# Kernel optimization log

Measured on AMD Instinct MI355X. Metric: run time of the kernel, lower is better.

The kernel has to match this reference:

```python
import jax, jax.numpy as jnp
import numpy as np

B, S, D = 2, 8192, 1024
H, DK, DV = 8, 64, 64
DH = 4096
SEG = 2048
NSEG = S // SEG
EPS = 1e-5


def setup_inputs() -> dict:
    key = jax.random.key(0)
    ks = jax.random.split(key, 9)
    g = lambda k, shp, sc: jax.random.normal(k, shp, jnp.float32) * sc
    return {
        "x": g(ks[0], (B, S, D), 1.0),
        "Wq": g(ks[1], (D, H * DK), 0.02),
        "Wk": g(ks[2], (D, H * DK), 0.02),
        "Wv": g(ks[3], (D, H * DV), 0.02),
        "Wo": g(ks[4], (H * DV, D), 0.02),
        "betas": g(ks[5], (1, H, 1, DV), 1.0),
        "W1": g(ks[6], (D, DH), 0.02),
        "b1": jnp.zeros((DH,), jnp.float32),
        "W2": g(ks[7], (DH, D), 0.02),
        "b2": jnp.zeros((D,), jnp.float32),
        "ln_g": jnp.ones((D,), jnp.float32),
        "ln_b": jnp.zeros((D,), jnp.float32),
    }


def _compressive_memory(x, Wq, Wk, Wv, Wo, betas):
    # project and split heads: (B, H, S, d)
    q = (x @ Wq).reshape(B, S, H, DK).transpose(0, 2, 1, 3)
    k = (x @ Wk).reshape(B, S, H, DK).transpose(0, 2, 1, 3)
    v = (x @ Wv).reshape(B, S, H, DV).transpose(0, 2, 1, 3)

    # chunk into segments: (NSEG, B, H, SEG, d)
    seg = lambda t, d: t.reshape(B, H, NSEG, SEG, d).transpose(2, 0, 1, 3, 4)
    qs, ks_, vs = seg(q, DK), seg(k, DK), seg(v, DV)

    mem0 = jnp.zeros((B, H, DK, DV), jnp.float32)
    z0 = jnp.ones((B, H, DK, 1), jnp.float32) / DK
    causal_mask = jnp.tril(jnp.ones((SEG, SEG), bool))
    scale = np.float32(1.0 / np.sqrt(DK))
    gate = jax.nn.sigmoid(betas)  # (1, H, 1, DV)

    def step(carry, inp):
        mem, z = carry
        qi, ki, vi = inp  # (B, H, SEG, d)
        sq = jax.nn.elu(qi) + 1.0
        sk = jax.nn.elu(ki) + 1.0
        # memory retrieval (uses state from previous segments)
        att_mem = (sq @ mem) / (sq @ z)  # (B, H, SEG, DV)
        # local causal SDP attention within the segment
        scores = jnp.einsum('bhqd,bhkd->bhqk', qi, ki) * scale
        scores = jnp.where(causal_mask, scores, -jnp.inf)
        att_dot = jax.nn.softmax(scores, axis=-1) @ vi
        # linear memory update
        mem = mem + jnp.einsum('bhsd,bhsv->bhdv', sk, vi)
        z = z + sk.sum(axis=-2, keepdims=True).transpose(0, 1, 3, 2)
        att = gate * att_mem + (1.0 - gate) * att_dot
        return (mem, z), att

    _, atts = jax.lax.scan(step, (mem0, z0), (qs, ks_, vs))
    # (NSEG, B, H, SEG, DV) -> (B, S, H*DV)
    att = atts.transpose(1, 0, 3, 2, 4).reshape(B, S, H * DV)
    return att @ Wo


def reference(x, Wq, Wk, Wv, Wo, betas, W1, b1, W2, b2, ln_g, ln_b):
    a = _compressive_memory(x, Wq, Wk, Wv, Wo, betas)
    h = jax.nn.gelu(a @ W1 + b1, approximate=False) @ W2 + b2
    y = h + x
    mu = y.mean(axis=-1, keepdims=True)
    var = ((y - mu) ** 2).mean(axis=-1, keepdims=True)
    return (y - mu) / jnp.sqrt(var + EPS) * ln_g + ln_b
```

## Files before the change

kernel.cpp:

```cpp
#include <hip/hip_runtime.h>
#include <hip/hip_bf16.h>
#include <math.h>

#define B_    2
#define S_    8192
#define D_    1024
#define H_N   8
#define DK_   64
#define DV_   64
#define DH_   4096
#define SEG_  2048
#define NSEG_ 4
#define EPS_  1e-5f
#define LDQKV 1536

typedef __hip_bfloat16 bf16;
typedef unsigned int u32;
typedef __attribute__((ext_vector_type(8))) short bf16x8;
typedef __attribute__((ext_vector_type(4))) float f32x4;

union bvec { bf16x8 v; bf16 e[8]; };

template <typename T> __device__ inline T from_f(float v);
template <> __device__ inline float from_f<float>(float v) { return v; }
template <> __device__ inline bf16  from_f<bf16>(float v)  { return __float2bfloat16(v); }

__device__ __forceinline__ void gld_lds16(const bf16* g, bf16* l) {
    __builtin_amdgcn_global_load_lds(
        (const __attribute__((address_space(1))) u32*)g,
        (__attribute__((address_space(3))) u32*)l, 16, 0, 0);
}

__device__ inline float elu1(float x) { return x > 0.f ? x + 1.f : __expf(x); }

template <int EPI, typename CT>
__global__ __launch_bounds__(512, 2) void gemm256(
    const bf16* __restrict__ A, const bf16* __restrict__ BT, CT* __restrict__ C,
    const float* __restrict__ bias, const float* __restrict__ resid,
    int M, int N, int K)
{
    __shared__ bf16 L[2][32768];
    const int t    = threadIdx.x;
    const int lane = t & 63;
    const int w    = t >> 6;
    const int la   = lane & 15;
    const int g    = lane >> 4;

    const int nx  = gridDim.x;
    const int nwg = nx * gridDim.y;
    const int lin = blockIdx.y * nx + blockIdx.x;
    const int swz = (lin & 7) * (nwg >> 3) + (lin >> 3);
    const int by  = swz / nx, bx = swz - by * nx;

    const int m0 = by * 256, n0 = bx * 256;
    const int wm = w >> 2, wn = w & 3;

    f32x4 acc[8][4];
    #pragma unroll
    for (int m = 0; m < 8; m++)
        #pragma unroll
        for (int n = 0; n < 4; n++) {
            f32x4 z4 = {0.f, 0.f, 0.f, 0.f};
            acc[m][n] = z4;
        }

    const bf16* Aw = A  + (size_t)(m0 + w * 32) * K;
    const bf16* Bw = BT + (size_t)(n0 + w * 32) * K;
    const int sr = lane >> 3;
    const int sc = ((lane & 7) ^ sr) * 8;

    const int nt = K >> 6;

    auto stage = [&](int kt) {
        const int buf = kt & 1;
        const size_t k0 = (size_t)kt << 6;
        #pragma unroll
        for (int i = 0; i < 4; i++) {
            gld_lds16(Aw + (size_t)(i * 8 + sr) * K + k0 + sc,
                      &L[buf][(w * 32 + i * 8) * 64]);
            gld_lds16(Bw + (size_t)(i * 8 + sr) * K + k0 + sc,
                      &L[buf][16384 + (w * 32 + i * 8) * 64]);
        }
    };

    auto rd = [&](const bf16* base, int row, int chunk) -> bf16x8 {
        return *(const bf16x8*)((const char*)base + row * 128 + ((chunk ^ (row & 7)) << 4));
    };

    stage(0);
    asm volatile("s_waitcnt vmcnt(0)" ::: "memory");
    __builtin_amdgcn_sched_barrier(0);
    __builtin_amdgcn_s_barrier();
    __builtin_amdgcn_sched_barrier(0);

    for (int kt = 0; kt < nt; kt++) {
        const bf16* Abuf = &L[kt & 1][0];
        const bf16* Bbuf = &L[kt & 1][16384];
        if (kt + 1 < nt) stage(kt + 1);

        #pragma unroll
        for (int ks = 0; ks < 2; ks++) {
            bf16x8 bg[4];
            #pragma unroll
            for (int n = 0; n < 4; n++)
                bg[n] = rd(Bbuf, wn * 64 + n * 16 + la, ks * 4 + g);
            #pragma unroll
            for (int mh = 0; mh < 2; mh++) {
                bf16x8 af[4];
                #pragma unroll
                for (int m = 0; m < 4; m++)
                    af[m] = rd(Abuf, wm * 128 + mh * 64 + m * 16 + la, ks * 4 + g);
                __builtin_amdgcn_s_setprio(1);
                #pragma unroll
                for (int m = 0; m < 4; m++)
                    #pragma unroll
                    for (int n = 0; n < 4; n++)
                        acc[mh * 4 + m][n] = __builtin_amdgcn_mfma_f32_16x16x32_bf16(
                            af[m], bg[n], acc[mh * 4 + m][n], 0, 0, 0);
                __builtin_amdgcn_s_setprio(0);
            }
        }

        if (kt + 1 < nt) {
            asm volatile("s_waitcnt vmcnt(0)" ::: "memory");
            __builtin_amdgcn_sched_barrier(0);
            __builtin_amdgcn_s_barrier();
            __builtin_amdgcn_sched_barrier(0);
        }
    }

    const int row0 = m0 + wm * 128 + g * 4;
    const int col0 = n0 + wn * 64 + la;
    #pragma unroll
    for (int n = 0; n < 4; n++) {
        const int col = col0 + n * 16;
        const float bj = (EPI >= 2) ? bias[col] : 0.f;
        #pragma unroll
        for (int m = 0; m < 8; m++) {
            #pragma unroll
            for (int r = 0; r < 4; r++) {
                const int row = row0 + m * 16 + r;
                float v = acc[m][n][r];
                if (EPI >= 2) v += bj;
                if (EPI == 2) v = 0.5f * v * (1.0f + erff(v * 0.70710678118654752f));
                if (EPI == 3) v += resid[(size_t)row * N + col];
                C[(size_t)row * N + col] = from_f<CT>(v);
            }
        }
    }
}

__global__ __launch_bounds__(256) void castx_k(const float* __restrict__ X,
                                               bf16* __restrict__ Y)
{
    size_t i = ((size_t)blockIdx.x * 256 + threadIdx.x) * 4;
    float4 v = *(const float4*)(X + i);
    union { bf16 b[4]; unsigned long long u; } o;
    o.b[0] = __float2bfloat16(v.x);
    o.b[1] = __float2bfloat16(v.y);
    o.b[2] = __float2bfloat16(v.z);
    o.b[3] = __float2bfloat16(v.w);
    *(unsigned long long*)(Y + i) = o.u;
}

__global__ __launch_bounds__(256) void transcast_k(const float* __restrict__ W,
                                                   bf16* __restrict__ WT, int K, int N)
{
    __shared__ float tile[32][33];
    const int n0 = blockIdx.x * 32, k0 = blockIdx.y * 32;
    const int tx = threadIdx.x & 31, ty = threadIdx.x >> 5;
    #pragma unroll
    for (int i = 0; i < 32; i += 8)
        tile[ty + i][tx] = W[(size_t)(k0 + ty + i) * N + n0 + tx];
    __syncthreads();
    #pragma unroll
    for (int i = 0; i < 32; i += 8)
        WT[(size_t)(n0 + ty + i) * K + k0 + tx] = __float2bfloat16(tile[tx][ty + i]);
}

__global__ __launch_bounds__(256) void vtrans_k(const bf16* __restrict__ V,
                                                bf16* __restrict__ Vt)
{
    __shared__ bf16 t_[64 * 64];
    const int t = threadIdx.x;
    const int sblk = blockIdx.x & 127;
    const int b = blockIdx.x >> 7;
    const int h = blockIdx.y;
    const bf16* src = V + ((size_t)b * S_ + sblk * 64) * LDQKV + h * 64;
    #pragma unroll
    for (int k = 0; k < 2; k++) {
        int e = t + k * 256;
        int r = e >> 3, c8 = (e & 7) * 8;
        *(bf16x8*)&t_[r * 64 + c8] = *(const bf16x8*)&src[(size_t)r * LDQKV + c8];
    }
    __syncthreads();
    const int dv = t & 63, s0 = (t >> 6) * 16;
    bf16* dst = Vt + ((size_t)(b * 8 + h) * 64 + dv) * (size_t)S_ + sblk * 64 + s0;
    bvec o0, o1;
    #pragma unroll
    for (int i = 0; i < 8; i++) {
        o0.e[i] = t_[(s0 + i) * 64 + dv];
        o1.e[i] = t_[(s0 + 8 + i) * 64 + dv];
    }
    *(bf16x8*)dst = o0.v;
    *(bf16x8*)(dst + 8) = o1.v;
}

__global__ __launch_bounds__(256) void memseg_k(
    const bf16* __restrict__ Kg, const bf16* __restrict__ Vg,
    float* __restrict__ MP, float* __restrict__ ZP)
{
    __shared__ float Ks[64][65];
    __shared__ float Vs[64][65];
    const int t = threadIdx.x, tx = t & 15, ty = t >> 4;
    const int sb = blockIdx.x;
    const int seg = sb >> 4, bh = sb & 15;
    const int b = bh >> 3, h = bh & 7;
    const int chunk = blockIdx.y;
    const size_t base = ((size_t)b * S_ + (size_t)seg * SEG_ + (size_t)chunk * 512) * LDQKV + h * 64;

    float acc[4][4] = {};
    float zacc[4]   = {};
    for (int st = 0; st < 8; st++) {
        #pragma unroll
        for (int kk = 0; kk < 2; kk++) {
            int e = t + kk * 256;
            int r = e >> 3, c8 = (e & 7) * 8;
            size_t go = base + ((size_t)st * 64 + r) * LDQKV + c8;
            bvec kv_, vv_;
            kv_.v = *(const bf16x8*)&Kg[go];
            vv_.v = *(const bf16x8*)&Vg[go];
            #pragma unroll
            for (int i = 0; i < 8; i++) {
                Ks[r][c8 + i] = elu1(__bfloat162float(kv_.e[i]));
                Vs[r][c8 + i] = __bfloat162float(vv_.e[i]);
            }
        }
        __syncthreads();
        for (int s = 0; s < 64; s++) {
            float a4[4], v4[4];
            #pragma unroll
            for (int i = 0; i < 4; i++) a4[i] = Ks[s][ty * 4 + i];
            #pragma unroll
            for (int j = 0; j < 4; j++) v4[j] = Vs[s][tx * 4 + j];
            #pragma unroll
            for (int i = 0; i < 4; i++)
                #pragma unroll
                for (int j = 0; j < 4; j++)
                    acc[i][j] += a4[i] * v4[j];
        }
        #pragma unroll
        for (int ii = 0; ii < 4; ii++) {
            int s = tx + ii * 16;
            #pragma unroll
            for (int i = 0; i < 4; i++) zacc[i] += Ks[s][ty * 4 + i];
        }
        __syncthreads();
    }
    const int slot = (seg * 4 + chunk) * 16 + bh;
    #pragma unroll
    for (int i = 0; i < 4; i++)
        #pragma unroll
        for (int j = 0; j < 4; j++)
            MP[(size_t)slot * 4096 + (ty * 4 + i) * 64 + tx * 4 + j] = acc[i][j];
    #pragma unroll
    for (int i = 0; i < 4; i++) {
        float zz = zacc[i];
        #pragma unroll
        for (int mk = 1; mk < 16; mk <<= 1) zz += __shfl_xor(zz, mk);
        if (tx == 0) ZP[slot * 64 + ty * 4 + i] = zz;
    }
}

__global__ __launch_bounds__(256) void prefix_k(
    const float* __restrict__ MP, const float* __restrict__ ZP,
    bf16* __restrict__ MST, float* __restrict__ ZS)
{
    const int bh = blockIdx.x, t = threadIdx.x;
    for (int e = t; e < 4096; e += 256) {
        int dk = e >> 6, dv = e & 63;
        float s = 0.f;
        #pragma unroll
        for (int slot = 0; slot < 16; slot++) {
            if ((slot & 3) == 0)
                MST[(size_t)((slot >> 2) * 16 + bh) * 4096 + dv * 64 + dk] = __float2bfloat16(s);
            s += MP[(size_t)(slot * 16 + bh) * 4096 + e];
        }
    }
    if (t < 64) {
        float s = 1.0f / DK_;
        #pragma unroll
        for (int slot = 0; slot < 16; slot++) {
            if ((slot & 3) == 0) ZS[((slot >> 2) * 16 + bh) * 64 + t] = s;
            s += ZP[(slot * 16 + bh) * 64 + t];
        }
    }
}

template <int NG>
__device__ __forceinline__ void stageT(const bf16* gsrc, size_t stride, bf16* lds,
                                       int wave, int lane)
{
    #pragma unroll
    for (int ii = 0; ii < NG; ii++) {
        int i = wave * NG + ii;
        gld_lds16(gsrc + (size_t)(8 * i + (lane >> 3)) * stride
                        + (size_t)(((lane & 7) ^ (lane >> 3)) * 8),
                  lds + i * 512);
    }
}

__device__ __forceinline__ bf16x8 ldsw128(const bf16* base, int row, int colE)
{
    int off = row * 128 + ((colE * 2) ^ ((row & 7) << 4));
    return *(const bf16x8*)((const char*)base + off);
}

__global__ __launch_bounds__(256) void attn_k(
    const bf16* __restrict__ Qg, const bf16* __restrict__ Kg, const bf16* __restrict__ Vt,
    const bf16* __restrict__ MsT, const float* __restrict__ ZS,
    const float* __restrict__ betas, bf16* __restrict__ att)
{
    __shared__ bf16 KT[2][4096];
    __shared__ bf16 VTs[2][4096];
    __shared__ bf16 QP[8192];
    __shared__ float Zsm[64];

    const int t    = threadIdx.x;
    const int lane = t & 63;
    const int w    = t >> 6;
    const int la   = lane & 15;
    const int g    = lane >> 4;
    const int qt   = (int)gridDim.x - 1 - (int)blockIdx.x;
    const int bh   = blockIdx.y;
    const int seg  = blockIdx.z;
    const int b    = bh >> 3, h = bh & 7;

    const size_t srow = (size_t)b * S_ + (size_t)seg * SEG_;
    const bf16* qp  = Qg + (srow + (size_t)qt * 128) * LDQKV + h * 64;
    const bf16* kp  = Kg + srow * LDQKV + h * 64;
    const bf16* vtp = Vt + (size_t)bh * 64 * (size_t)S_ + (size_t)seg * SEG_;

    stageT<4>(qp, LDQKV, QP, w, lane);
    stageT<2>(kp, LDQKV, KT[0], w, lane);
    stageT<2>(vtp, S_, VTs[0], w, lane);
    if (t < 64) Zsm[t] = ZS[(seg * 16 + bh) * 64 + t];
    __syncthreads();

    bf16x8 aq[2][2];
    #pragma unroll
    for (int st = 0; st < 2; st++)
        #pragma unroll
        for (int s = 0; s < 2; s++)
            aq[st][s] = ldsw128(QP, w * 32 + st * 16 + la, s * 32 + g * 8);

    float m_[2] = {-1e30f, -1e30f};
    float l_[2] = {0.f, 0.f};
    f32x4 Oa[2][4];
    #pragma unroll
    for (int st = 0; st < 2; st++)
        #pragma unroll
        for (int j = 0; j < 4; j++) { f32x4 z4 = {0.f,0.f,0.f,0.f}; Oa[st][j] = z4; }

    const int jtmax = 2 * qt + 1;
    int cur = 0;
    for (int jt = 0; jt <= jtmax; jt++, cur ^= 1) {
        if (jt < jtmax) {
            stageT<2>(kp + (size_t)(jt + 1) * 64 * LDQKV, LDQKV, KT[cur ^ 1], w, lane);
            stageT<2>(vtp + (size_t)(jt + 1) * 64, S_, VTs[cur ^ 1], w, lane);
        }

        bf16x8 kf[2][4];
        #pragma unroll
        for (int s = 0; s < 2; s++)
            #pragma unroll
            for (int j = 0; j < 4; j++)
                kf[s][j] = ldsw128(KT[cur], j * 16 + la, s * 32 + g * 8);

        const int jtkv = jt * 64;
        #pragma unroll
        for (int st = 0; st < 2; st++) {
            f32x4 sc[4];
            #pragma unroll
            for (int j = 0; j < 4; j++) { f32x4 z4 = {0.f,0.f,0.f,0.f}; sc[j] = z4; }
            #pragma unroll
            for (int j = 0; j < 4; j++) {
                sc[j] = __builtin_amdgcn_mfma_f32_16x16x32_bf16(kf[0][j], aq[st][0], sc[j], 0, 0, 0);
                sc[j] = __builtin_amdgcn_mfma_f32_16x16x32_bf16(kf[1][j], aq[st][1], sc[j], 0, 0, 0);
            }

            const int q_abs = qt * 128 + w * 32 + st * 16 + la;
            float sv[4][4];
            float mx = -1e30f;
            #pragma unroll
            for (int j = 0; j < 4; j++)
                #pragma unroll
                for (int r = 0; r < 4; r++) {
                    float v = sc[j][r] * 0.125f;
                    int kv = jtkv + j * 16 + g * 4 + r;
                    v = (kv <= q_abs) ? v : -1e30f;
                    sv[j][r] = v;
                    mx = fmaxf(mx, v);
                }
            mx = fmaxf(mx, __shfl_xor(mx, 16));
            mx = fmaxf(mx, __shfl_xor(mx, 32));
            float mnew = fmaxf(m_[st], mx);
            float corr = __expf(m_[st] - mnew);
            float rs = 0.f;
            #pragma unroll
            for (int j = 0; j < 4; j++)
                #pragma unroll
                for (int r = 0; r < 4; r++) {
                    float p = __expf(sv[j][r] - mnew);
                    sv[j][r] = p;
                    rs += p;
                }
            rs += __shfl_xor(rs, 16);
            rs += __shfl_xor(rs, 32);
            l_[st] = l_[st] * corr + rs;
            m_[st] = mnew;

            const int R = w * 32 + st * 16 + la;
            #pragma unroll
            for (int j = 0; j < 4; j++) {
                union { bf16 e[4]; uint2 u; } pk;
                #pragma unroll
                for (int r = 0; r < 4; r++) pk.e[r] = __float2bfloat16(sv[j][r]);
                int off = R * 128 + ((j * 32 + g * 8) ^ ((la & 7) << 4));
                *(uint2*)((char*)QP + off) = pk.u;
            }

            #pragma unroll
            for (int r = 0; r < 4; r++) {
                float corr_r = __shfl(corr, (lane & 48) | (g * 4 + r));
                #pragma unroll
                for (int j = 0; j < 4; j++) Oa[st][j][r] *= corr_r;
            }
        }

        asm volatile("s_waitcnt lgkmcnt(0)" ::: "memory");
        __builtin_amdgcn_sched_barrier(0);

        bf16x8 bv[2][4];
        #pragma unroll
        for (int s = 0; s < 2; s++)
            #pragma unroll
            for (int j = 0; j < 4; j++)
                bv[s][j] = ldsw128(VTs[cur], j * 16 + la, s * 32 + g * 8);
        #pragma unroll
        for (int st = 0; st < 2; st++) {
            bf16x8 ap0 = ldsw128(QP, w * 32 + st * 16 + la, g * 8);
            bf16x8 ap1 = ldsw128(QP, w * 32 + st * 16 + la, 32 + g * 8);
            #pragma unroll
            for (int j = 0; j < 4; j++) {
                Oa[st][j] = __builtin_amdgcn_mfma_f32_16x16x32_bf16(ap0, bv[0][j], Oa[st][j], 0, 0, 0);
                Oa[st][j] = __builtin_amdgcn_mfma_f32_16x16x32_bf16(ap1, bv[1][j], Oa[st][j], 0, 0, 0);
            }
        }
        __syncthreads();
    }

    stageT<2>(MsT + (size_t)(seg * 16 + bh) * 4096, 64, KT[0], w, lane);
    __syncthreads();

    bf16x8 sq[2][2];
    float den[2] = {0.f, 0.f};
    #pragma unroll
    for (int st = 0; st < 2; st++) {
        #pragma unroll
        for (int s = 0; s < 2; s++) {
            bvec in, outv;
            in.v = aq[st][s];
            #pragma unroll
            for (int e = 0; e < 8; e++) {
                float f = elu1(__bfloat162float(in.e[e]));
                outv.e[e] = __float2bfloat16(f);
                den[st] += f * Zsm[s * 32 + 8 * g + e];
            }
            sq[st][s] = outv.v;
        }
        den[st] += __shfl_xor(den[st], 16);
        den[st] += __shfl_xor(den[st], 32);
    }

    bf16x8 bm[2][4];
    #pragma unroll
    for (int s = 0; s < 2; s++)
        #pragma unroll
        for (int j = 0; j < 4; j++)
            bm[s][j] = ldsw128(KT[0], j * 16 + la, s * 32 + g * 8);

    float gate[4];
    #pragma unroll
    for (int j = 0; j < 4; j++)
        gate[j] = 1.f / (1.f + __expf(-betas[h * 64 + j * 16 + la]));

    #pragma unroll
    for (int st = 0; st < 2; st++) {
        f32x4 num[4];
        #pragma unroll
        for (int j = 0; j < 4; j++) { f32x4 z4 = {0.f,0.f,0.f,0.f}; num[j] = z4; }
        #pragma unroll
        for (int j = 0; j < 4; j++) {
            num[j] = __builtin_amdgcn_mfma_f32_16x16x32_bf16(sq[st][0], bm[0][j], num[j], 0, 0, 0);
            num[j] = __builtin_amdgcn_mfma_f32_16x16x32_bf16(sq[st][1], bm[1][j], num[j], 0, 0, 0);
        }
        #pragma unroll
        for (int r = 0; r < 4; r++) {
            float den_r = __shfl(den[st], (lane & 48) | (g * 4 + r));
            float l_r   = __shfl(l_[st],  (lane & 48) | (g * 4 + r));
            float linv  = 1.f / l_r;
            float dinv  = 1.f / den_r;
            size_t orow = srow + (size_t)qt * 128 + w * 32 + st * 16 + g * 4 + r;
            #pragma unroll
            for (int j = 0; j < 4; j++) {
                float am = num[j][r] * dinv;
                float ad = Oa[st][j][r] * linv;
                att[orow * 512 + h * 64 + j * 16 + la] =
                    __float2bfloat16(gate[j] * am + (1.f - gate[j]) * ad);
            }
        }
    }
}

__global__ __launch_bounds__(256) void ln_k(
    const float* __restrict__ Y, const float* __restrict__ g,
    const float* __restrict__ bta, float* __restrict__ out)
{
    const int row = blockIdx.x;
    const float* yp = Y + (size_t)row * D_;
    const int t = threadIdx.x;
    float v[4];
    float s = 0.f, s2 = 0.f;
    #pragma unroll
    for (int i = 0; i < 4; i++) {
        v[i] = yp[t + i * 256];
        s += v[i]; s2 += v[i] * v[i];
    }
    #pragma unroll
    for (int mk = 1; mk < 64; mk <<= 1) {
        s  += __shfl_xor(s, mk);
        s2 += __shfl_xor(s2, mk);
    }
    __shared__ float ss[4], ss2[4];
    int w = t >> 6;
    if ((t & 63) == 0) { ss[w] = s; ss2[w] = s2; }
    __syncthreads();
    s  = ss[0] + ss[1] + ss[2] + ss[3];
    s2 = ss2[0] + ss2[1] + ss2[2] + ss2[3];
    float mu   = s / D_;
    float var  = s2 / D_ - mu * mu;
    float rstd = rsqrtf(var + EPS_);
    #pragma unroll
    for (int i = 0; i < 4; i++) {
        int c = t + i * 256;
        out[(size_t)row * D_ + c] = (v[i] - mu) * rstd * g[c] + bta[c];
    }
}

extern "C" void kernel_launch(void* const* d_in, const int* in_sizes, int n_in,
                              void* d_out, int out_size, void* d_ws, size_t ws_size,
                              hipStream_t stream)
{
    const float* x     = (const float*)d_in[0];
    const float* Wq    = (const float*)d_in[1];
    const float* Wk    = (const float*)d_in[2];
    const float* Wv    = (const float*)d_in[3];
    const float* Wo    = (const float*)d_in[4];
    const float* betas = (const float*)d_in[5];
    const float* W1    = (const float*)d_in[6];
    const float* b1    = (const float*)d_in[7];
    const float* W2    = (const float*)d_in[8];
    const float* b2    = (const float*)d_in[9];
    const float* lng   = (const float*)d_in[10];
    const float* lnb   = (const float*)d_in[11];
    float* out = (float*)d_out;

    const int M = B_ * S_;
    char* base = (char*)d_ws;
    const size_t MB = 1024 * 1024;

    bf16*  Ab    = (bf16*)(base);
    bf16*  Hb    = (bf16*)(base + 32 * MB);
    bf16*  Xbf   = (bf16*)(base + 32 * MB);
    bf16*  QKV   = (bf16*)(base + 64 * MB);
    bf16*  Vt    = (bf16*)(base + 112 * MB);
    bf16*  ATT   = (bf16*)(base + 128 * MB);
    bf16*  WqkvT = (bf16*)(base + 160 * MB);
    bf16*  WoT   = (bf16*)(base + 163 * MB);
    bf16*  W1T   = (bf16*)(base + 164 * MB);
    bf16*  W2T   = (bf16*)(base + 172 * MB);
    float* MP    = (float*)(base + 180 * MB);
    bf16*  MST   = (bf16*)(base + 184 * MB);
    float* ZP    = (float*)(base + 185 * MB);
    float* ZS    = (float*)(base + 185 * MB + 256 * 1024);

    dim3 blk(256);
    dim3 blk512(512);

    castx_k<<<dim3((M * D_) / 1024), blk, 0, stream>>>(x, Xbf);
    transcast_k<<<dim3(512 / 32, 1024 / 32), blk, 0, stream>>>(Wq, WqkvT, 1024, 512);
    transcast_k<<<dim3(512 / 32, 1024 / 32), blk, 0, stream>>>(Wk, WqkvT + 512 * 1024, 1024, 512);
    transcast_k<<<dim3(512 / 32, 1024 / 32), blk, 0, stream>>>(Wv, WqkvT + 1024 * 1024, 1024, 512);
    transcast_k<<<dim3(1024 / 32, 512 / 32), blk, 0, stream>>>(Wo, WoT, 512, 1024);
    transcast_k<<<dim3(4096 / 32, 1024 / 32), blk, 0, stream>>>(W1, W1T, 1024, 4096);
    transcast_k<<<dim3(1024 / 32, 4096 / 32), blk, 0, stream>>>(W2, W2T, 4096, 1024);

    gemm256<0, bf16><<<dim3(1536 / 256, M / 256), blk512, 0, stream>>>(
        Xbf, WqkvT, QKV, nullptr, nullptr, M, 1536, 1024);

    vtrans_k<<<dim3(256, 8), blk, 0, stream>>>(QKV + 1024, Vt);

    memseg_k<<<dim3(NSEG_ * 16, 4), blk, 0, stream>>>(QKV + 512, QKV + 1024, MP, ZP);
    prefix_k<<<dim3(16), blk, 0, stream>>>(MP, ZP, MST, ZS);

    attn_k<<<dim3(SEG_ / 128, 16, NSEG_), blk, 0, stream>>>(
        QKV, QKV + 512, Vt, MST, ZS, betas, ATT);

    gemm256<0, bf16><<<dim3(1024 / 256, M / 256), blk512, 0, stream>>>(
        ATT, WoT, Ab, nullptr, nullptr, M, 1024, 512);
    gemm256<2, bf16><<<dim3(4096 / 256, M / 256), blk512, 0, stream>>>(
        Ab, W1T, Hb, b1, nullptr, M, 4096, 1024);
    gemm256<3, float><<<dim3(1024 / 256, M / 256), blk512, 0, stream>>>(
        Hb, W2T, out, b2, x, M, 1024, 4096);

    ln_k<<<dim3(M), blk, 0, stream>>>(out, lng, lnb, out);
}
```

Measured before the change: 702.4 us.

## Split GEMM k-step into four phases interleaving prefetch with MFMA clusters

Restructures the 256x256 GEMM main loop into four phases per k-tile. Each phase loads a quarter of the next tile into LDS, reads its fragments, and runs a 4x4 MFMA cluster, with barriers between phases so global-to-LDS traffic overlaps compute more evenly. It also changes launch bounds from 2 to 1 blocks per CU, allowing more registers per thread at the cost of occupancy. The epilogue is reordered to hoist bias loads and iterate columns innermost. The extra barriers add synchronization overhead.

```diff
diff --git a/kernel.cpp b/kernel.cpp
--- a/kernel.cpp
+++ b/kernel.cpp
@@ -34,7 +34,7 @@
 __device__ inline float elu1(float x) { return x > 0.f ? x + 1.f : __expf(x); }
 
 template <int EPI, typename CT>
-__global__ __launch_bounds__(512, 2) void gemm256(
+__global__ __launch_bounds__(512, 1) void gemm256(
     const bf16* __restrict__ A, const bf16* __restrict__ BT, CT* __restrict__ C,
     const float* __restrict__ bias, const float* __restrict__ resid,
     int M, int N, int K)
@@ -64,84 +64,131 @@
             acc[m][n] = z4;
         }
 
-    const bf16* Aw = A  + (size_t)(m0 + w * 32) * K;
-    const bf16* Bw = BT + (size_t)(n0 + w * 32) * K;
-    const int sr = lane >> 3;
-    const int sc = ((lane & 7) ^ sr) * 8;
-
     const int nt = K >> 6;
 
-    auto stage = [&](int kt) {
-        const int buf = kt & 1;
-        const size_t k0 = (size_t)kt << 6;
-        #pragma unroll
-        for (int i = 0; i < 4; i++) {
-            gld_lds16(Aw + (size_t)(i * 8 + sr) * K + k0 + sc,
-                      &L[buf][(w * 32 + i * 8) * 64]);
-            gld_lds16(Bw + (size_t)(i * 8 + sr) * K + k0 + sc,
-                      &L[buf][16384 + (w * 32 + i * 8) * 64]);
-        }
+    auto stageQ = [&](int kt_, int q) {
+        const int buf = kt_ & 1;
+        const size_t k0 = (size_t)kt_ << 6;
+        const int rq = w * 8 + (lane >> 3);
+        const int c8 = ((lane & 7) ^ (lane >> 3)) * 8;
+        gld_lds16(A  + (size_t)(m0 + q * 64 + rq) * K + k0 + c8,
+                  &L[buf][q * 4096 + w * 512]);
+        gld_lds16(BT + (size_t)(n0 + q * 64 + rq) * K + k0 + c8,
+                  &L[buf][16384 + q * 4096 + w * 512]);
     };
 
-    auto rd = [&](const bf16* base, int row, int chunk) -> bf16x8 {
-        return *(const bf16x8*)((const char*)base + row * 128 + ((chunk ^ (row & 7)) << 4));
-    };
-
-    stage(0);
+    stageQ(0, 0); stageQ(0, 1); stageQ(0, 2); stageQ(0, 3);
     asm volatile("s_waitcnt vmcnt(0)" ::: "memory");
     __builtin_amdgcn_sched_barrier(0);
     __builtin_amdgcn_s_barrier();
     __builtin_amdgcn_sched_barrier(0);
 
     for (int kt = 0; kt < nt; kt++) {
-        const bf16* Abuf = &L[kt & 1][0];
-        const bf16* Bbuf = &L[kt & 1][16384];
-        if (kt + 1 < nt) stage(kt + 1);
-
-        #pragma unroll
-        for (int ks = 0; ks < 2; ks++) {
-            bf16x8 bg[4];
+        const bf16* Ab_ = &L[kt & 1][0];
+        const bf16* Bb_ = &L[kt & 1][16384];
+        const bool pre = (kt + 1 < nt);
+        bf16x8 af[4], bg[4];
+
+        auto rdA = [&](int m, int ks) -> bf16x8 {
+            int row = wm * 128 + m * 16 + la;
+            return *(const bf16x8*)((const char*)Ab_ + row * 128
+                                    + (((ks * 4 + g) ^ (row & 7)) << 4));
+        };
+        auto rdB = [&](int n, int ks) -> bf16x8 {
+            int row = wn * 64 + n * 16 + la;
+            return *(const bf16x8*)((const char*)Bb_ + row * 128
+                                    + (((ks * 4 + g) ^ (row & 7)) << 4));
+        };
+
+        #pragma unroll
+        for (int n = 0; n < 4; n++) bg[n] = rdB(n, 0);
+        #pragma unroll
+        for (int m = 0; m < 4; m++) af[m] = rdA(m, 0);
+        if (pre) stageQ(kt + 1, 0);
+        __builtin_amdgcn_s_barrier();
+        asm volatile("s_waitcnt lgkmcnt(0)" ::: "memory");
+        __builtin_amdgcn_sched_barrier(0);
+        __builtin_amdgcn_s_setprio(1);
+        #pragma unroll
+        for (int m = 0; m < 4; m++)
             #pragma unroll
             for (int n = 0; n < 4; n++)
-                bg[n] = rd(Bbuf, wn * 64 + n * 16 + la, ks * 4 + g);
-            #pragma unroll
-            for (int mh = 0; mh < 2; mh++) {
-                bf16x8 af[4];
-                #pragma unroll
-                for (int m = 0; m < 4; m++)
-                    af[m] = rd(Abuf, wm * 128 + mh * 64 + m * 16 + la, ks * 4 + g);
-                __builtin_amdgcn_s_setprio(1);
-                #pragma unroll
-                for (int m = 0; m < 4; m++)
-                    #pragma unroll
-                    for (int n = 0; n < 4; n++)
-                        acc[mh * 4 + m][n] = __builtin_amdgcn_mfma_f32_16x16x32_bf16(
-                            af[m], bg[n], acc[mh * 4 + m][n], 0, 0, 0);
-                __builtin_amdgcn_s_setprio(0);
-            }
-        }
-
-        if (kt + 1 < nt) {
-            asm volatile("s_waitcnt vmcnt(0)" ::: "memory");
-            __builtin_amdgcn_sched_barrier(0);
-            __builtin_amdgcn_s_barrier();
-            __builtin_amdgcn_sched_barrier(0);
-        }
+                acc[m][n] = __builtin_amdgcn_mfma_f32_16x16x32_bf16(
+                    af[m], bg[n], acc[m][n], 0, 0, 0);
+        __builtin_amdgcn_s_setprio(0);
+        __builtin_amdgcn_s_barrier();
+
+        #pragma unroll
+        for (int m = 0; m < 4; m++) af[m] = rdA(4 + m, 0);
+        if (pre) stageQ(kt + 1, 1);
+        __builtin_amdgcn_s_barrier();
+        asm volatile("s_waitcnt lgkmcnt(0)" ::: "memory");
+        __builtin_amdgcn_sched_barrier(0);
+        __builtin_amdgcn_s_setprio(1);
+        #pragma unroll
+        for (int m = 0; m < 4; m++)
+            #pragma unroll
+            for (int n = 0; n < 4; n++)
+                acc[4 + m][n] = __builtin_amdgcn_mfma_f32_16x16x32_bf16(
+                    af[m], bg[n], acc[4 + m][n], 0, 0, 0);
+        __builtin_amdgcn_s_setprio(0);
+        __builtin_amdgcn_s_barrier();
+
+        #pragma unroll
+        for (int n = 0; n < 4; n++) bg[n] = rdB(n, 1);
+        #pragma unroll
+        for (int m = 0; m < 4; m++) af[m] = rdA(m, 1);
+        if (pre) stageQ(kt + 1, 2);
+        __builtin_amdgcn_s_barrier();
+        asm volatile("s_waitcnt lgkmcnt(0)" ::: "memory");
+        __builtin_amdgcn_sched_barrier(0);
+        __builtin_amdgcn_s_setprio(1);
+        #pragma unroll
+        for (int m = 0; m < 4; m++)
+            #pragma unroll
+            for (int n = 0; n < 4; n++)
+                acc[m][n] = __builtin_amdgcn_mfma_f32_16x16x32_bf16(
+                    af[m], bg[n], acc[m][n], 0, 0, 0);
+        __builtin_amdgcn_s_setprio(0);
+        __builtin_amdgcn_s_barrier();
+
+        #pragma unroll
+        for (int m = 0; m < 4; m++) af[m] = rdA(4 + m, 1);
+        if (pre) stageQ(kt + 1, 3);
+        __builtin_amdgcn_s_barrier();
+        asm volatile("s_waitcnt lgkmcnt(0)" ::: "memory");
+        __builtin_amdgcn_sched_barrier(0);
+        __builtin_amdgcn_s_setprio(1);
+        #pragma unroll
+        for (int m = 0; m < 4; m++)
+            #pragma unroll
+            for (int n = 0; n < 4; n++)
+                acc[4 + m][n] = __builtin_amdgcn_mfma_f32_16x16x32_bf16(
+                    af[m], bg[n], acc[4 + m][n], 0, 0, 0);
+        __builtin_amdgcn_s_setprio(0);
+        if (pre) asm volatile("s_waitcnt vmcnt(0)" ::: "memory");
+        __builtin_amdgcn_sched_barrier(0);
+        __builtin_amdgcn_s_barrier();
+        __builtin_amdgcn_sched_barrier(0);
     }
 
     const int row0 = m0 + wm * 128 + g * 4;
     const int col0 = n0 + wn * 64 + la;
-    #pragma unroll
-    for (int n = 0; n < 4; n++) {
-        const int col = col0 + n * 16;
-        const float bj = (EPI >= 2) ? bias[col] : 0.f;
-        #pragma unroll
-        for (int m = 0; m < 8; m++) {
-            #pragma unroll
-            for (int r = 0; r < 4; r++) {
-                const int row = row0 + m * 16 + r;
+    float bj[4];
+    if (EPI >= 2) {
+        #pragma unroll
+        for (int n = 0; n < 4; n++) bj[n] = bias[col0 + n * 16];
+    }
+    #pragma unroll
+    for (int m = 0; m < 8; m++) {
+        #pragma unroll
+        for (int r = 0; r < 4; r++) {
+            const int row = row0 + m * 16 + r;
+            #pragma unroll
+            for (int n = 0; n < 4; n++) {
+                const int col = col0 + n * 16;
                 float v = acc[m][n][r];
-                if (EPI >= 2) v += bj;
+                if (EPI >= 2) v += bj[n];
                 if (EPI == 2) v = 0.5f * v * (1.0f + erff(v * 0.70710678118654752f));
                 if (EPI == 3) v += resid[(size_t)row * N + col];
                 C[(size_t)row * N + col] = from_f<CT>(v);
```

Result: no change. 701.1 us (-0.2%).

## Restructure GEMM main loop with quarter-tile staged loads interleaved with MFMA phases

Applied to the files above, without the earlier changes.

Rewrites the bf16 GEMM inner loop to unroll two k-tiles at once with separate LDS buffers. Each buffer is loaded in four quarter-tile chunks that are issued between MFMA phases and gated by partial vmcnt waits and barriers. LDS read addresses are precomputed per buffer, and launch bounds drop to one workgroup per CU. The goal is finer-grained overlap of global-to-LDS traffic with matrix math. The cost is many more barriers per iteration and lower occupancy. The epilogue loop order is also changed and the bias loads are hoisted.

```diff
diff --git a/kernel.cpp b/kernel.cpp
--- a/kernel.cpp
+++ b/kernel.cpp
@@ -33,13 +33,36 @@
 
 __device__ inline float elu1(float x) { return x > 0.f ? x + 1.f : __expf(x); }
 
+#define GP(APTR, BPTR, MH, LOADB)                                              \
+    {                                                                          \
+        if (LOADB) {                                                           \
+            _Pragma("unroll")                                                  \
+            for (int n = 0; n < 4; n++)                                        \
+                bg[n] = *(const bf16x8*)((BPTR) + n * 2048);                   \
+        }                                                                      \
+        _Pragma("unroll")                                                      \
+        for (int m = 0; m < 4; m++)                                            \
+            af[m] = *(const bf16x8*)((APTR) + (MH) * 8192 + m * 2048);         \
+        asm volatile("s_waitcnt lgkmcnt(0)" ::: "memory");                     \
+        __builtin_amdgcn_sched_barrier(0);                                     \
+        __builtin_amdgcn_s_setprio(1);                                         \
+        _Pragma("unroll")                                                      \
+        for (int m = 0; m < 4; m++)                                            \
+            _Pragma("unroll")                                                  \
+            for (int n = 0; n < 4; n++)                                        \
+                acc[(MH) * 4 + m][n] = __builtin_amdgcn_mfma_f32_16x16x32_bf16(\
+                    af[m], bg[n], acc[(MH) * 4 + m][n], 0, 0, 0);              \
+        __builtin_amdgcn_s_setprio(0);                                         \
+    }
+
 template <int EPI, typename CT>
-__global__ __launch_bounds__(512, 2) void gemm256(
+__global__ __launch_bounds__(512, 1) void gemm256(
     const bf16* __restrict__ A, const bf16* __restrict__ BT, CT* __restrict__ C,
     const float* __restrict__ bias, const float* __restrict__ resid,
     int M, int N, int K)
 {
-    __shared__ bf16 L[2][32768];
+    __shared__ bf16 L0[32768];
+    __shared__ bf16 L1[32768];
     const int t    = threadIdx.x;
     const int lane = t & 63;
     const int w    = t >> 6;
@@ -49,8 +72,8 @@
     const int nx  = gridDim.x;
     const int nwg = nx * gridDim.y;
     const int lin = blockIdx.y * nx + blockIdx.x;
-    const int swz = (lin & 7) * (nwg >> 3) + (lin >> 3);
-    const int by  = swz / nx, bx = swz - by * nx;
+    const int swzb = (lin & 7) * (nwg >> 3) + (lin >> 3);
+    const int by  = swzb / nx, bx = swzb - by * nx;
 
     const int m0 = by * 256, n0 = bx * 256;
     const int wm = w >> 2, wn = w & 3;
@@ -64,84 +87,89 @@
             acc[m][n] = z4;
         }
 
-    const bf16* Aw = A  + (size_t)(m0 + w * 32) * K;
-    const bf16* Bw = BT + (size_t)(n0 + w * 32) * K;
-    const int sr = lane >> 3;
-    const int sc = ((lane & 7) ^ sr) * 8;
-
     const int nt = K >> 6;
 
-    auto stage = [&](int kt) {
-        const int buf = kt & 1;
-        const size_t k0 = (size_t)kt << 6;
-        #pragma unroll
-        for (int i = 0; i < 4; i++) {
-            gld_lds16(Aw + (size_t)(i * 8 + sr) * K + k0 + sc,
-                      &L[buf][(w * 32 + i * 8) * 64]);
-            gld_lds16(Bw + (size_t)(i * 8 + sr) * K + k0 + sc,
-                      &L[buf][16384 + (w * 32 + i * 8) * 64]);
-        }
+    const int rq = w * 8 + (lane >> 3);
+    const int c8 = ((lane & 7) ^ (lane >> 3)) * 8;
+    auto stageQ = [&](int kt_, int q, bf16* Lb) {
+        const size_t k0 = (size_t)kt_ << 6;
+        gld_lds16(A  + (size_t)(m0 + q * 64 + rq) * K + k0 + c8,
+                  Lb + q * 4096 + w * 512);
+        gld_lds16(BT + (size_t)(n0 + q * 64 + rq) * K + k0 + c8,
+                  Lb + 16384 + q * 4096 + w * 512);
     };
 
-    auto rd = [&](const bf16* base, int row, int chunk) -> bf16x8 {
-        return *(const bf16x8*)((const char*)base + row * 128 + ((chunk ^ (row & 7)) << 4));
-    };
-
-    stage(0);
-    asm volatile("s_waitcnt vmcnt(0)" ::: "memory");
-    __builtin_amdgcn_sched_barrier(0);
-    __builtin_amdgcn_s_barrier();
-    __builtin_amdgcn_sched_barrier(0);
-
-    for (int kt = 0; kt < nt; kt++) {
-        const bf16* Abuf = &L[kt & 1][0];
-        const bf16* Bbuf = &L[kt & 1][16384];
-        if (kt + 1 < nt) stage(kt + 1);
-
-        #pragma unroll
-        for (int ks = 0; ks < 2; ks++) {
-            bf16x8 bg[4];
-            #pragma unroll
-            for (int n = 0; n < 4; n++)
-                bg[n] = rd(Bbuf, wn * 64 + n * 16 + la, ks * 4 + g);
-            #pragma unroll
-            for (int mh = 0; mh < 2; mh++) {
-                bf16x8 af[4];
-                #pragma unroll
-                for (int m = 0; m < 4; m++)
-                    af[m] = rd(Abuf, wm * 128 + mh * 64 + m * 16 + la, ks * 4 + g);
-                __builtin_amdgcn_s_setprio(1);
-                #pragma unroll
-                for (int m = 0; m < 4; m++)
-                    #pragma unroll
-                    for (int n = 0; n < 4; n++)
-                        acc[mh * 4 + m][n] = __builtin_amdgcn_mfma_f32_16x16x32_bf16(
-                            af[m], bg[n], acc[mh * 4 + m][n], 0, 0, 0);
-                __builtin_amdgcn_s_setprio(0);
-            }
-        }
-
-        if (kt + 1 < nt) {
+    const int sw0 = (g ^ (la & 7)) << 4;
+    const int sw1 = ((4 + g) ^ (la & 7)) << 4;
+    const int aoff = (wm * 128 + la) * 128;
+    const int boff = 32768 + (wn * 64 + la) * 128;
+    const char* a0k0 = (const char*)L0 + aoff + sw0;
+    const char* a0k1 = (const char*)L0 + aoff + sw1;
+    const char* b0k0 = (const char*)L0 + boff + sw0;
+    const char* b0k1 = (const char*)L0 + boff + sw1;
+    const char* a1k0 = (const char*)L1 + aoff + sw0;
+    const char* a1k1 = (const char*)L1 + aoff + sw1;
+    const char* b1k0 = (const char*)L1 + boff + sw0;
+    const char* b1k1 = (const char*)L1 + boff + sw1;
+
+    stageQ(0, 0, L0); stageQ(0, 1, L0); stageQ(0, 2, L0); stageQ(0, 3, L0);
+
+    bf16x8 af[4], bg[4];
+    for (int tt = 0; tt < nt; tt += 2) {
+        const bool more = (tt + 2 < nt);
+        __builtin_amdgcn_s_barrier();
+        stageQ(tt + 1, 0, L1);
+        asm volatile("s_waitcnt vmcnt(2)" ::: "memory");
+        __builtin_amdgcn_sched_barrier(0);
+        __builtin_amdgcn_s_barrier();
+        GP(a0k0, b0k0, 0, true);
+        __builtin_amdgcn_s_barrier();
+        stageQ(tt + 1, 1, L1);
+        GP(a0k0, b0k0, 1, false);
+        __builtin_amdgcn_s_barrier();
+        stageQ(tt + 1, 2, L1);
+        GP(a0k1, b0k1, 0, true);
+        __builtin_amdgcn_s_barrier();
+        stageQ(tt + 1, 3, L1);
+        GP(a0k1, b0k1, 1, false);
+        __builtin_amdgcn_s_barrier();
+        if (more) {
+            stageQ(tt + 2, 0, L0);
+            asm volatile("s_waitcnt vmcnt(2)" ::: "memory");
+        } else {
             asm volatile("s_waitcnt vmcnt(0)" ::: "memory");
-            __builtin_amdgcn_sched_barrier(0);
-            __builtin_amdgcn_s_barrier();
-            __builtin_amdgcn_sched_barrier(0);
-        }
+        }
+        __builtin_amdgcn_sched_barrier(0);
+        __builtin_amdgcn_s_barrier();
+        GP(a1k0, b1k0, 0, true);
+        __builtin_amdgcn_s_barrier();
+        if (more) stageQ(tt + 2, 1, L0);
+        GP(a1k0, b1k0, 1, false);
+        __builtin_amdgcn_s_barrier();
+        if (more) stageQ(tt + 2, 2, L0);
+        GP(a1k1, b1k1, 0, true);
+        __builtin_amdgcn_s_barrier();
+        if (more) stageQ(tt + 2, 3, L0);
+        GP(a1k1, b1k1, 1, false);
     }
 
     const int row0 = m0 + wm * 128 + g * 4;
     const int col0 = n0 + wn * 64 + la;
-    #pragma unroll
-    for (int n = 0; n < 4; n++) {
-        const int col = col0 + n * 16;
-        const float bj = (EPI >= 2) ? bias[col] : 0.f;
-        #pragma unroll
-        for (int m = 0; m < 8; m++) {
-            #pragma unroll
-            for (int r = 0; r < 4; r++) {
-                const int row = row0 + m * 16 + r;
+    float bj[4];
+    if (EPI >= 2) {
+        #pragma unroll
+        for (int n = 0; n < 4; n++) bj[n] = bias[col0 + n * 16];
+    }
+    #pragma unroll
+    for (int m = 0; m < 8; m++) {
+        #pragma unroll
+        for (int r = 0; r < 4; r++) {
+            const int row = row0 + m * 16 + r;
+            #pragma unroll
+            for (int n = 0; n < 4; n++) {
+                const int col = col0 + n * 16;
                 float v = acc[m][n][r];
-                if (EPI >= 2) v += bj;
+                if (EPI >= 2) v += bj[n];
                 if (EPI == 2) v = 0.5f * v * (1.0f + erff(v * 0.70710678118654752f));
                 if (EPI == 3) v += resid[(size_t)row * N + col];
                 C[(size_t)row * N + col] = from_f<CT>(v);
```

New measurement: 699.7 us. Within noise of the previous version (-0.4%).

## Restructure GEMM main loop into finer-grained staged pipeline with barrier-interleaved MFMA

Applied to the files above, without the earlier changes.

Rewrites the 256x256 GEMM inner loop to stage each K-tile in four sub-units split by k-half and operand. It unrolls two K-tiles per iteration over explicit L0/L1 buffers and interleaves global-to-LDS loads, LDS reads and MFMA blocks with partial vmcnt waits and extra barriers. The LDS layout and swizzle are changed to match the 32-wide k-halves, and occupancy is lowered to one workgroup per CU. The aim is to overlap memory traffic with MFMA more tightly, at the cost of many more barriers and reduced occupancy.

```diff
diff --git a/kernel.cpp b/kernel.cpp
--- a/kernel.cpp
+++ b/kernel.cpp
@@ -33,13 +33,34 @@
 
 __device__ inline float elu1(float x) { return x > 0.f ? x + 1.f : __expf(x); }
 
+#define RD_B(BASE)                                                             \
+    { _Pragma("unroll") for (int n = 0; n < 4; n++)                            \
+        bg[n] = *(const bf16x8*)((BASE) + n * 1024); }
+#define RD_A(BASE, MH)                                                         \
+    { _Pragma("unroll") for (int m = 0; m < 4; m++)                            \
+        af[m] = *(const bf16x8*)((BASE) + (MH) * 4096 + m * 1024); }
+#define MFMAQ(MH)                                                              \
+    __builtin_amdgcn_s_barrier();                                              \
+    asm volatile("s_waitcnt lgkmcnt(0)" ::: "memory");                         \
+    __builtin_amdgcn_sched_barrier(0);                                         \
+    __builtin_amdgcn_s_setprio(1);                                             \
+    _Pragma("unroll")                                                          \
+    for (int m = 0; m < 4; m++)                                                \
+        _Pragma("unroll")                                                      \
+        for (int n = 0; n < 4; n++)                                            \
+            acc[(MH) * 4 + m][n] = __builtin_amdgcn_mfma_f32_16x16x32_bf16(    \
+                af[m], bg[n], acc[(MH) * 4 + m][n], 0, 0, 0);                  \
+    __builtin_amdgcn_s_setprio(0);
+#define VMC(N) asm volatile("s_waitcnt vmcnt(" #N ")" ::: "memory")
+
 template <int EPI, typename CT>
-__global__ __launch_bounds__(512, 2) void gemm256(
+__global__ __launch_bounds__(512, 1) void gemm256(
     const bf16* __restrict__ A, const bf16* __restrict__ BT, CT* __restrict__ C,
     const float* __restrict__ bias, const float* __restrict__ resid,
     int M, int N, int K)
 {
-    __shared__ bf16 L[2][32768];
+    __shared__ bf16 L0[32768];
+    __shared__ bf16 L1[32768];
     const int t    = threadIdx.x;
     const int lane = t & 63;
     const int w    = t >> 6;
@@ -49,8 +70,8 @@
     const int nx  = gridDim.x;
     const int nwg = nx * gridDim.y;
     const int lin = blockIdx.y * nx + blockIdx.x;
-    const int swz = (lin & 7) * (nwg >> 3) + (lin >> 3);
-    const int by  = swz / nx, bx = swz - by * nx;
+    const int swzb = (lin & 7) * (nwg >> 3) + (lin >> 3);
+    const int by  = swzb / nx, bx = swzb - by * nx;
 
     const int m0 = by * 256, n0 = bx * 256;
     const int wm = w >> 2, wn = w & 3;
@@ -64,84 +85,102 @@
             acc[m][n] = z4;
         }
 
-    const bf16* Aw = A  + (size_t)(m0 + w * 32) * K;
-    const bf16* Bw = BT + (size_t)(n0 + w * 32) * K;
-    const int sr = lane >> 3;
-    const int sc = ((lane & 7) ^ sr) * 8;
-
     const int nt = K >> 6;
 
-    auto stage = [&](int kt) {
-        const int buf = kt & 1;
-        const size_t k0 = (size_t)kt << 6;
-        #pragma unroll
-        for (int i = 0; i < 4; i++) {
-            gld_lds16(Aw + (size_t)(i * 8 + sr) * K + k0 + sc,
-                      &L[buf][(w * 32 + i * 8) * 64]);
-            gld_lds16(Bw + (size_t)(i * 8 + sr) * K + k0 + sc,
-                      &L[buf][16384 + (w * 32 + i * 8) * 64]);
+    const int srow_ = lane >> 2;
+    const int sc8   = ((lane & 3) ^ ((lane >> 3) & 3)) * 8;
+    auto stageU = [&](int kt_, int u, bf16* Lb) {
+        const int  ks  = u >> 1;
+        const bool isA = (u & 1);
+        const bf16* src = isA ? (A + (size_t)m0 * K) : (BT + (size_t)n0 * K);
+        bf16* dst = Lb + (isA ? 0 : 16384) + ks * 8192;
+        const size_t kb = ((size_t)kt_ << 6) + ks * 32;
+        #pragma unroll
+        for (int j = 0; j < 2; j++) {
+            const int row = (j * 8 + w) * 16 + srow_;
+            gld_lds16(src + (size_t)row * K + kb + sc8, dst + (j * 8 + w) * 512);
         }
     };
 
-    auto rd = [&](const bf16* base, int row, int chunk) -> bf16x8 {
-        return *(const bf16x8*)((const char*)base + row * 128 + ((chunk ^ (row & 7)) << 4));
-    };
-
-    stage(0);
-    asm volatile("s_waitcnt vmcnt(0)" ::: "memory");
+    const int rsw = (la >> 1) & 3;
+    const char* a0k[2]; const char* b0k[2]; const char* a1k[2]; const char* b1k[2];
+    #pragma unroll
+    for (int ks = 0; ks < 2; ks++) {
+        const int aoff = ks * 16384 + (wm * 128 + la) * 64 + ((g ^ rsw) << 4);
+        const int boff = 32768 + ks * 16384 + (wn * 64 + la) * 64 + ((g ^ rsw) << 4);
+        a0k[ks] = (const char*)L0 + aoff;  b0k[ks] = (const char*)L0 + boff;
+        a1k[ks] = (const char*)L1 + aoff;  b1k[ks] = (const char*)L1 + boff;
+    }
+
+    stageU(0, 0, L0); stageU(0, 1, L0); stageU(0, 2, L0); stageU(0, 3, L0);
+    VMC(6);
     __builtin_amdgcn_sched_barrier(0);
     __builtin_amdgcn_s_barrier();
-    __builtin_amdgcn_sched_barrier(0);
-
-    for (int kt = 0; kt < nt; kt++) {
-        const bf16* Abuf = &L[kt & 1][0];
-        const bf16* Bbuf = &L[kt & 1][16384];
-        if (kt + 1 < nt) stage(kt + 1);
-
-        #pragma unroll
-        for (int ks = 0; ks < 2; ks++) {
-            bf16x8 bg[4];
-            #pragma unroll
-            for (int n = 0; n < 4; n++)
-                bg[n] = rd(Bbuf, wn * 64 + n * 16 + la, ks * 4 + g);
-            #pragma unroll
-            for (int mh = 0; mh < 2; mh++) {
-                bf16x8 af[4];
-                #pragma unroll
-                for (int m = 0; m < 4; m++)
-                    af[m] = rd(Abuf, wm * 128 + mh * 64 + m * 16 + la, ks * 4 + g);
-                __builtin_amdgcn_s_setprio(1);
-                #pragma unroll
-                for (int m = 0; m < 4; m++)
-                    #pragma unroll
-                    for (int n = 0; n < 4; n++)
-                        acc[mh * 4 + m][n] = __builtin_amdgcn_mfma_f32_16x16x32_bf16(
-                            af[m], bg[n], acc[mh * 4 + m][n], 0, 0, 0);
-                __builtin_amdgcn_s_setprio(0);
-            }
-        }
-
-        if (kt + 1 < nt) {
-            asm volatile("s_waitcnt vmcnt(0)" ::: "memory");
+
+    bf16x8 af[4], bg[4];
+    for (int tt = 0; tt < nt; tt += 2) {
+        const bool more = (tt + 2 < nt);
+        stageU(tt + 1, 0, L1);
+        RD_B(b0k[0]); RD_A(a0k[0], 0);
+        MFMAQ(0);
+        __builtin_amdgcn_s_barrier();
+        RD_A(a0k[0], 1);
+        stageU(tt + 1, 1, L1);
+        MFMAQ(1);
+        VMC(6);
+        __builtin_amdgcn_sched_barrier(0);
+        __builtin_amdgcn_s_barrier();
+        stageU(tt + 1, 2, L1);
+        RD_B(b0k[1]); RD_A(a0k[1], 0);
+        MFMAQ(0);
+        __builtin_amdgcn_s_barrier();
+        RD_A(a0k[1], 1);
+        stageU(tt + 1, 3, L1);
+        MFMAQ(1);
+        VMC(6);
+        __builtin_amdgcn_sched_barrier(0);
+        __builtin_amdgcn_s_barrier();
+        if (more) stageU(tt + 2, 0, L0);
+        RD_B(b1k[0]); RD_A(a1k[0], 0);
+        MFMAQ(0);
+        __builtin_amdgcn_s_barrier();
+        RD_A(a1k[0], 1);
+        if (more) stageU(tt + 2, 1, L0);
+        MFMAQ(1);
+        if (more) { VMC(6); } else { VMC(0); }
+        __builtin_amdgcn_sched_barrier(0);
+        __builtin_amdgcn_s_barrier();
+        if (more) stageU(tt + 2, 2, L0);
+        RD_B(b1k[1]); RD_A(a1k[1], 0);
+        MFMAQ(0);
+        __builtin_amdgcn_s_barrier();
+        RD_A(a1k[1], 1);
+        if (more) stageU(tt + 2, 3, L0);
+        MFMAQ(1);
+        if (more) {
+            VMC(6);
             __builtin_amdgcn_sched_barrier(0);
-            __builtin_amdgcn_s_barrier();
-            __builtin_amdgcn_sched_barrier(0);
-        }
+        }
+        __builtin_amdgcn_s_barrier();
     }
 
     const int row0 = m0 + wm * 128 + g * 4;
     const int col0 = n0 + wn * 64 + la;
-    #pragma unroll
-    for (int n = 0; n < 4; n++) {
-        const int col = col0 + n * 16;
-        const float bj = (EPI >= 2) ? bias[col] : 0.f;
-        #pragma unroll
-        for (int m = 0; m < 8; m++) {
-            #pragma unroll
-            for (int r = 0; r < 4; r++) {
-                const int row = row0 + m * 16 + r;
+    float bj[4];
+    if (EPI >= 2) {
+        #pragma unroll
+        for (int n = 0; n < 4; n++) bj[n] = bias[col0 + n * 16];
+    }
+    #pragma unroll
+    for (int m = 0; m < 8; m++) {
+        #pragma unroll
+        for (int r = 0; r < 4; r++) {
+            const int row = row0 + m * 16 + r;
+            #pragma unroll
+            for (int n = 0; n < 4; n++) {
+                const int col = col0 + n * 16;
                 float v = acc[m][n][r];
-                if (EPI >= 2) v += bj;
+                if (EPI >= 2) v += bj[n];
                 if (EPI == 2) v = 0.5f * v * (1.0f + erff(v * 0.70710678118654752f));
                 if (EPI == 3) v += resid[(size_t)row * N + col];
                 C[(size_t)row * N + col] = from_f<CT>(v);
```

Measured after the change: 714.9 us. Within noise of the previous version (+1.8%).
